# Kernel tuning notes

Hardware: AMD Instinct MI355X
Metric: run time of the kernel (lower is better)

The kernel has to match this reference:

```python
import jax, jax.numpy as jnp
import numpy as np

DIM = 64          # d_model
D_INNER = 128     # 2 * DIM (mamba expand=2)
D_STATE = 16
D_CONV = 4
DT_RANK = 4       # ceil(DIM / 16)


def setup_inputs() -> dict:
    key = jax.random.key(0)
    ks = jax.random.split(key, 8)
    s = 0.05
    f32 = jnp.float32
    return {
        "x": jax.random.normal(ks[0], (2, DIM, 96, 96), f32),
        # GroupNorm(1, dim)
        "gn_gamma": jnp.ones((DIM,), f32),
        "gn_beta": jnp.zeros((DIM,), f32),
        # Mamba params
        "W_in": (jax.random.normal(ks[1], (2 * D_INNER, DIM), f32) * s),
        "b_in": jnp.zeros((2 * D_INNER,), f32),
        "conv_w": (jax.random.normal(ks[2], (D_INNER, 1, D_CONV), f32) * s),
        "conv_b": jnp.zeros((D_INNER,), f32),
        "W_xproj": (jax.random.normal(ks[3], (DT_RANK + 2 * D_STATE, D_INNER), f32) * s),
        "W_dt": (jax.random.normal(ks[4], (D_INNER, DT_RANK), f32) * s),
        "b_dt": jnp.full((D_INNER,), -4.6, f32),  # softplus(-4.6) ~ 0.01
        "A_log": jnp.log(jnp.broadcast_to(jnp.arange(1, D_STATE + 1, dtype=f32), (D_INNER, D_STATE))),
        "Dp": jnp.ones((D_INNER,), f32),
        "W_out": (jax.random.normal(ks[5], (DIM, D_INNER), f32) * s),
        "b_out": jnp.zeros((DIM,), f32),
        # proj: Conv2d(dim, dim, 1) + BatchNorm2d(dim) eval-mode + GELU
        "proj_w": (jax.random.normal(ks[6], (DIM, DIM), f32) * s),
        "proj_b": jnp.zeros((DIM,), f32),
        "bn_gamma": jnp.ones((DIM,), f32),
        "bn_beta": jnp.zeros((DIM,), f32),
        "bn_mean": jnp.zeros((DIM,), f32),
        "bn_var": jnp.ones((DIM,), f32),
    }


def _mamba(u, W_in, b_in, conv_w, conv_b, W_xproj, W_dt, b_dt, A_log, Dp, W_out, b_out):
    # u: [B, L, DIM]
    xz = u @ W_in.T + b_in                      # [B, L, 2*D_INNER]
    x, z = jnp.split(xz, 2, axis=-1)            # each [B, L, D_INNER]
    # depthwise causal conv over L
    xc = jnp.transpose(x, (0, 2, 1))            # [B, D_INNER, L]
    xc = jax.lax.conv_general_dilated(
        xc, conv_w, (1,), [(D_CONV - 1, 0)],
        dimension_numbers=("NCH", "OIH", "NCH"), feature_group_count=D_INNER)
    x = jax.nn.silu(jnp.transpose(xc, (0, 2, 1)) + conv_b)   # [B, L, D_INNER]
    # input-dependent dt, B, C
    dbc = x @ W_xproj.T                          # [B, L, DT_RANK + 2*D_STATE]
    dt = dbc[..., :DT_RANK]
    Bm = dbc[..., DT_RANK:DT_RANK + D_STATE]     # [B, L, D_STATE]
    Cm = dbc[..., DT_RANK + D_STATE:]            # [B, L, D_STATE]
    dt = jax.nn.softplus(dt @ W_dt.T + b_dt)     # [B, L, D_INNER]
    A = -jnp.exp(A_log)                          # [D_INNER, D_STATE]
    deltaA = jnp.exp(dt[..., None] * A)                          # [B, L, D_INNER, D_STATE]
    deltaBu = dt[..., None] * Bm[:, :, None, :] * x[..., None]   # [B, L, D_INNER, D_STATE]
    # parallel linear recurrence h_t = a_t * h_{t-1} + b_t, h_0 = 0
    def comb(e1, e2):
        a1, b1 = e1
        a2, b2 = e2
        return a1 * a2, a2 * b1 + b2
    _, h = jax.lax.associative_scan(comb, (deltaA, deltaBu), axis=1)
    y = jnp.einsum("blds,bls->bld", h, Cm) + x * Dp
    y = y * jax.nn.silu(z)
    return y @ W_out.T + b_out                   # [B, L, DIM]


def reference(x, gn_gamma, gn_beta, W_in, b_in, conv_w, conv_b, W_xproj, W_dt, b_dt,
              A_log, Dp, W_out, b_out, proj_w, proj_b, bn_gamma, bn_beta, bn_mean, bn_var):
    B, C, H, W = x.shape
    # GroupNorm(1, C): normalize over (C, H, W) per sample, biased var
    mu = x.mean(axis=(1, 2, 3), keepdims=True)
    var = x.var(axis=(1, 2, 3), keepdims=True)
    xn = (x - mu) / jnp.sqrt(var + 1e-5)
    xn = xn * gn_gamma[None, :, None, None] + gn_beta[None, :, None, None]
    xn = jnp.clip(xn, -10.0, 10.0)
    res = xn
    seq = jnp.transpose(xn, (0, 2, 3, 1)).reshape(B, H * W, C)
    y = _mamba(seq, W_in, b_in, conv_w, conv_b, W_xproj, W_dt, b_dt, A_log, Dp, W_out, b_out)
    y2d = jnp.transpose(y.reshape(B, H, W, C), (0, 3, 1, 2))
    # proj: 1x1 conv + eval BatchNorm + exact GELU
    p = jnp.einsum("oc,bchw->bohw", proj_w, y2d) + proj_b[None, :, None, None]
    p = (p - bn_mean[None, :, None, None]) / jnp.sqrt(bn_var[None, :, None, None] + 1e-5)
    p = p * bn_gamma[None, :, None, None] + bn_beta[None, :, None, None]
    p = jax.nn.gelu(p, approximate=False)
    return jnp.clip(res + p, -10.0, 10.0)
```

## Files before the change

kernel.cpp:

```cpp
#include <hip/hip_runtime.h>
#include <math.h>

#define DIMC 64
#define DIN  128
#define LSEQ 9216
#define NPB  (DIMC*LSEQ)
#define NCH  192
#define CTL  48
#define NCHAIN 4096
#define PADR 132

__device__ __forceinline__ float siluf(float v)    { return v / (1.f + __expf(-v)); }
__device__ __forceinline__ float softplusf(float v){ return (v > 20.f) ? v : log1pf(__expf(v)); }
__device__ __forceinline__ float clip10(float v)   { return fminf(10.f, fmaxf(-10.f, v)); }

__global__ void k_reduce(const float* __restrict__ x, float* __restrict__ sums) {
  int b = blockIdx.y;
  const float* xb = x + (size_t)b * NPB;
  float s = 0.f, s2 = 0.f;
  for (int i = blockIdx.x * blockDim.x + threadIdx.x; i < NPB; i += gridDim.x * blockDim.x) {
    float v = xb[i]; s += v; s2 = fmaf(v, v, s2);
  }
  __shared__ float l1[256], l2[256];
  int t = threadIdx.x;
  l1[t] = s; l2[t] = s2; __syncthreads();
  for (int off = 128; off > 0; off >>= 1) {
    if (t < off) { l1[t] += l1[t + off]; l2[t] += l2[t + off]; }
    __syncthreads();
  }
  if (t == 0) { atomicAdd(&sums[2*b], l1[0]); atomicAdd(&sums[2*b+1], l2[0]); }
}

__global__ void k_norm(const float* __restrict__ x, const float* __restrict__ gam,
                       const float* __restrict__ bet, const float* __restrict__ sums,
                       float* __restrict__ seq, float* __restrict__ res) {
  int b = blockIdx.y, l0 = blockIdx.x * 64;
  float mean = sums[2*b] * (1.f / NPB);
  float var  = sums[2*b+1] * (1.f / NPB) - mean * mean;
  float inv  = rsqrtf(var + 1e-5f);
  __shared__ float tile[64][65];
  int t = threadIdx.x;
  int lr = t & 63, cg = t >> 6;
  #pragma unroll
  for (int i = 0; i < 16; i++) {
    int c = i * 4 + cg;
    size_t idx = ((size_t)(b * DIMC + c)) * LSEQ + l0 + lr;
    float v = x[idx];
    v = (v - mean) * inv * gam[c] + bet[c];
    v = clip10(v);
    res[idx] = v;
    tile[c][lr] = v;
  }
  __syncthreads();
  int cc = t & 63, lg = t >> 6;
  #pragma unroll
  for (int i = 0; i < 16; i++) {
    int l = i * 4 + lg;
    seq[((size_t)(b * LSEQ + l0 + l)) * DIMC + cc] = tile[cc][l];
  }
}

__global__ void k_prep(const float* __restrict__ W_in, const float* __restrict__ proj_w,
                       const float* __restrict__ W_out, const float* __restrict__ b_out,
                       const float* __restrict__ proj_b,
                       float* __restrict__ Wt, float* __restrict__ Mt, float* __restrict__ bp) {
  int i = blockIdx.x * 256 + threadIdx.x;
  if (i < 16384) {
    int k = i >> 8, c = i & 255;
    Wt[i] = W_in[c * 64 + k];
    return;
  }
  int j = i - 16384;
  if (j < 8192) {
    int d = j >> 6, o = j & 63;
    float a = 0.f;
    for (int c = 0; c < 64; c++) a = fmaf(proj_w[o * 64 + c], W_out[c * DIN + d], a);
    Mt[j] = a;
    return;
  }
  int k2 = i - 24576;
  if (k2 < 64) {
    float a = proj_b[k2];
    for (int c = 0; c < 64; c++) a = fmaf(proj_w[k2 * 64 + c], b_out[c], a);
    bp[k2] = a;
  }
}

__global__ void k_inproj(const float* __restrict__ seq, const float* __restrict__ Wt,
                         const float* __restrict__ b_in,
                         float* __restrict__ xo, float* __restrict__ zo) {
  int row0 = blockIdx.x * 16;
  int c = threadIdx.x;
  float acc[16];
  float bi = b_in[c];
  #pragma unroll
  for (int r = 0; r < 16; r++) acc[r] = bi;
  const float* sp = seq + (size_t)row0 * DIMC;
  #pragma unroll 4
  for (int k = 0; k < 64; k++) {
    float w = Wt[k * 256 + c];
    #pragma unroll
    for (int r = 0; r < 16; r++) acc[r] = fmaf(w, sp[r * 64 + k], acc[r]);
  }
  #pragma unroll
  for (int r = 0; r < 16; r++) {
    size_t rr = (size_t)(row0 + r);
    if (c < DIN) xo[rr * DIN + c] = acc[r];
    else         zo[rr * DIN + (c - DIN)] = acc[r];
  }
}

__global__ void k_conv_proj(const float* __restrict__ x, const float* __restrict__ conv_w,
                            const float* __restrict__ conv_b, const float* __restrict__ W_xproj,
                            const float* __restrict__ W_dt, const float* __restrict__ b_dt,
                            float* __restrict__ xs, float* __restrict__ dt,
                            float* __restrict__ Bm, float* __restrict__ Cm) {
  int b = blockIdx.y, l0 = blockIdx.x * 64;
  __shared__ float xt[67 * PADR];
  __shared__ float red[4 * 64 * 37];
  __shared__ float dt4[64 * 4];
  int t = threadIdx.x;

  for (int i = t; i < 67 * 128; i += 256) {
    int lr = i >> 7, d = i & 127;
    int l = l0 - 3 + lr;
    xt[lr * PADR + d] = (l >= 0) ? x[((size_t)b * LSEQ + l) * DIN + d] : 0.f;
  }
  __syncthreads();

  int q = t >> 6;
  int qu = __builtin_amdgcn_readfirstlane(q);
  int lr = t & 63;
  size_t row = (size_t)b * LSEQ + l0 + lr;
  const float* xtr = xt + lr * PADR + qu * 32;
  const float4* cw4 = (const float4*)conv_w;
  const float4* cb4 = (const float4*)conv_b;
  float xv[32];
  #pragma unroll
  for (int c = 0; c < 8; c++) {
    int dbase = qu * 32 + c * 4;
    float4 t0 = *(const float4*)(xtr + 0 * PADR + c * 4);
    float4 t1 = *(const float4*)(xtr + 1 * PADR + c * 4);
    float4 t2 = *(const float4*)(xtr + 2 * PADR + c * 4);
    float4 t3 = *(const float4*)(xtr + 3 * PADR + c * 4);
    float4 cb = cb4[qu * 8 + c];
    float4 w;
    float a0, a1, a2, a3;
    w = cw4[dbase + 0];
    a0 = cb.x; a0 = fmaf(t0.x, w.x, a0); a0 = fmaf(t1.x, w.y, a0);
    a0 = fmaf(t2.x, w.z, a0); a0 = fmaf(t3.x, w.w, a0); a0 = siluf(a0);
    w = cw4[dbase + 1];
    a1 = cb.y; a1 = fmaf(t0.y, w.x, a1); a1 = fmaf(t1.y, w.y, a1);
    a1 = fmaf(t2.y, w.z, a1); a1 = fmaf(t3.y, w.w, a1); a1 = siluf(a1);
    w = cw4[dbase + 2];
    a2 = cb.z; a2 = fmaf(t0.z, w.x, a2); a2 = fmaf(t1.z, w.y, a2);
    a2 = fmaf(t2.z, w.z, a2); a2 = fmaf(t3.z, w.w, a2); a2 = siluf(a2);
    w = cw4[dbase + 3];
    a3 = cb.w; a3 = fmaf(t0.w, w.x, a3); a3 = fmaf(t1.w, w.y, a3);
    a3 = fmaf(t2.w, w.z, a3); a3 = fmaf(t3.w, w.w, a3); a3 = siluf(a3);
    xv[c * 4 + 0] = a0; xv[c * 4 + 1] = a1; xv[c * 4 + 2] = a2; xv[c * 4 + 3] = a3;
    *(float4*)(xs + row * DIN + dbase) = make_float4(a0, a1, a2, a3);
  }

  const float4* W4 = (const float4*)W_xproj;
  float* myred = red + (q * 64 + lr) * 37;
  for (int j = 0; j < 36; j++) {
    const float4* wr = W4 + j * 32 + qu * 8;
    float p0 = 0.f, p1 = 0.f;
    #pragma unroll
    for (int c = 0; c < 8; c += 2) {
      float4 w0 = wr[c], w1 = wr[c + 1];
      p0 = fmaf(xv[c * 4 + 0], w0.x, p0);
      p0 = fmaf(xv[c * 4 + 1], w0.y, p0);
      p0 = fmaf(xv[c * 4 + 2], w0.z, p0);
      p0 = fmaf(xv[c * 4 + 3], w0.w, p0);
      p1 = fmaf(xv[c * 4 + 4], w1.x, p1);
      p1 = fmaf(xv[c * 4 + 5], w1.y, p1);
      p1 = fmaf(xv[c * 4 + 6], w1.z, p1);
      p1 = fmaf(xv[c * 4 + 7], w1.w, p1);
    }
    myred[j] = p0 + p1;
  }
  __syncthreads();

  for (int k = 0; k < 9; k++) {
    int task = t + k * 256;
    int lrr = task / 36, j = task - lrr * 36;
    int o = lrr * 37 + j;
    float ssum = red[o] + red[2368 + o] + red[2 * 2368 + o] + red[3 * 2368 + o];
    size_t rrow = (size_t)b * LSEQ + l0 + lrr;
    if (j < 4)       dt4[lrr * 4 + j] = ssum;
    else if (j < 20) Bm[rrow * 16 + (j - 4)]  = ssum;
    else             Cm[rrow * 16 + (j - 20)] = ssum;
  }
  __syncthreads();

  int lr2 = t >> 2, q2 = t & 3;
  float4 dv = *(const float4*)(dt4 + lr2 * 4);
  size_t rrow = (size_t)b * LSEQ + l0 + lr2;
  const float4* Wd4 = (const float4*)W_dt;
  const float4* bd4 = (const float4*)b_dt;
  #pragma unroll
  for (int c = 0; c < 8; c++) {
    int dd = q2 * 32 + c * 4;
    float4 bb = bd4[q2 * 8 + c];
    float4 w;
    float s0, s1, s2, s3;
    w = Wd4[dd + 0];
    s0 = bb.x; s0 = fmaf(dv.x, w.x, s0); s0 = fmaf(dv.y, w.y, s0);
    s0 = fmaf(dv.z, w.z, s0); s0 = fmaf(dv.w, w.w, s0);
    w = Wd4[dd + 1];
    s1 = bb.y; s1 = fmaf(dv.x, w.x, s1); s1 = fmaf(dv.y, w.y, s1);
    s1 = fmaf(dv.z, w.z, s1); s1 = fmaf(dv.w, w.w, s1);
    w = Wd4[dd + 2];
    s2 = bb.z; s2 = fmaf(dv.x, w.x, s2); s2 = fmaf(dv.y, w.y, s2);
    s2 = fmaf(dv.z, w.z, s2); s2 = fmaf(dv.w, w.w, s2);
    w = Wd4[dd + 3];
    s3 = bb.w; s3 = fmaf(dv.x, w.x, s3); s3 = fmaf(dv.y, w.y, s3);
    s3 = fmaf(dv.z, w.z, s3); s3 = fmaf(dv.w, w.w, s3);
    *(float4*)(dt + rrow * DIN + dd) =
        make_float4(softplusf(s0), softplusf(s1), softplusf(s2), softplusf(s3));
  }
}

__global__ void __launch_bounds__(512) k_scanA(
    const float* __restrict__ dt, const float* __restrict__ Bmat,
    const float* __restrict__ xs, const float* __restrict__ A_log,
    float* __restrict__ Ap, float* __restrict__ Bg) {
  int chunk = blockIdx.x, b = blockIdx.y;
  int t = threadIdx.x;
  int d = t >> 2, q = t & 3;
  const float* al = A_log + d * 16 + q * 4;
  float a0 = -__expf(al[0]), a1 = -__expf(al[1]);
  float a2 = -__expf(al[2]), a3 = -__expf(al[3]);
  size_t base = (size_t)b * LSEQ + (size_t)chunk * CTL;
  const float* dtp = dt + base * DIN + d;
  const float* xsp = xs + base * DIN + d;
  const float4* bp4 = (const float4*)(Bmat + base * 16 + q * 4);
  float h0 = 0.f, h1 = 0.f, h2 = 0.f, h3 = 0.f;
  float p0 = 1.f, p1 = 1.f, p2 = 1.f, p3 = 1.f;
  #pragma unroll 4
  for (int i = 0; i < CTL; i++) {
    float dtv = dtp[(size_t)i * DIN];
    float xv  = xsp[(size_t)i * DIN];
    float4 bA = bp4[i * 4];
    float u = dtv * xv;
    float e;
    e = __expf(dtv * a0); h0 = fmaf(e, h0, u * bA.x); p0 *= e;
    e = __expf(dtv * a1); h1 = fmaf(e, h1, u * bA.y); p1 *= e;
    e = __expf(dtv * a2); h2 = fmaf(e, h2, u * bA.z); p2 *= e;
    e = __expf(dtv * a3); h3 = fmaf(e, h3, u * bA.w); p3 *= e;
  }
  size_t idx = (size_t)chunk * NCHAIN + (size_t)(b * DIN + d) * 16 + q * 4;
  *(float4*)(Ap + idx) = make_float4(p0, p1, p2, p3);
  *(float4*)(Bg + idx) = make_float4(h0, h1, h2, h3);
}

__global__ void k_scanB(const float* __restrict__ Ap, const float* __restrict__ Bg,
                        float* __restrict__ hinit) {
  int chain = blockIdx.x * 64 + threadIdx.x;
  float h = 0.f;
  for (int c = 0; c < NCH; c++) {
    size_t idx = (size_t)c * NCHAIN + chain;
    hinit[idx] = h;
    h = fmaf(Ap[idx], h, Bg[idx]);
  }
}

__global__ void __launch_bounds__(512) k_scanC(
    const float* __restrict__ dt, const float* __restrict__ Bmat,
    const float* __restrict__ Cmat, const float* __restrict__ xs,
    const float* __restrict__ z, const float* __restrict__ A_log,
    const float* __restrict__ Dp, const float* __restrict__ hinit,
    float* __restrict__ y) {
  int chunk = blockIdx.x, b = blockIdx.y;
  int t = threadIdx.x;
  int d = t >> 2, q = t & 3;
  const float* al = A_log + d * 16 + q * 4;
  float a0 = -__expf(al[0]), a1 = -__expf(al[1]);
  float a2 = -__expf(al[2]), a3 = -__expf(al[3]);
  float dp = Dp[d];
  size_t base = (size_t)b * LSEQ + (size_t)chunk * CTL;
  const float* dtp = dt + base * DIN + d;
  const float* xsp = xs + base * DIN + d;
  const float* zp  = z  + base * DIN + d;
  float* yp        = y  + base * DIN + d;
  const float4* bp4 = (const float4*)(Bmat + base * 16 + q * 4);
  const float4* cp4 = (const float4*)(Cmat + base * 16 + q * 4);
  size_t idx = (size_t)chunk * NCHAIN + (size_t)(b * DIN + d) * 16 + q * 4;
  float4 hv = *(const float4*)(hinit + idx);
  float h0 = hv.x, h1 = hv.y, h2 = hv.z, h3 = hv.w;
  #pragma unroll 2
  for (int i = 0; i < CTL; i++) {
    float dtv = dtp[(size_t)i * DIN];
    float xv  = xsp[(size_t)i * DIN];
    float4 bA = bp4[i * 4];
    float4 cA = cp4[i * 4];
    float u = dtv * xv;
    float e, p;
    e = __expf(dtv * a0); h0 = fmaf(e, h0, u * bA.x); p  = h0 * cA.x;
    e = __expf(dtv * a1); h1 = fmaf(e, h1, u * bA.y); p  = fmaf(h1, cA.y, p);
    e = __expf(dtv * a2); h2 = fmaf(e, h2, u * bA.z); p  = fmaf(h2, cA.z, p);
    e = __expf(dtv * a3); h3 = fmaf(e, h3, u * bA.w); p  = fmaf(h3, cA.w, p);
    p += __shfl_xor(p, 1);
    p += __shfl_xor(p, 2);
    if (q == 0) {
      float zv = zp[(size_t)i * DIN];
      yp[(size_t)i * DIN] = (p + xv * dp) * siluf(zv);
    }
  }
}

__global__ void k_out(const float* __restrict__ y, const float* __restrict__ Mt,
                      const float* __restrict__ bp, const float* __restrict__ bn_g,
                      const float* __restrict__ bn_bt, const float* __restrict__ bn_m,
                      const float* __restrict__ bn_v, const float* __restrict__ res,
                      float* __restrict__ out) {
  int b = blockIdx.y, l0 = blockIdx.x * 64;
  int t = threadIdx.x;
  int c = t & 63, lg = t >> 6;
  __shared__ float tile[64][65];
  float acc[16];
  float bpc = bp[c];
  #pragma unroll
  for (int i = 0; i < 16; i++) acc[i] = bpc;
  const float* yb = y + ((size_t)b * LSEQ + l0 + lg * 16) * DIN;
  #pragma unroll 4
  for (int d = 0; d < DIN; d++) {
    float m = Mt[d * 64 + c];
    #pragma unroll
    for (int i = 0; i < 16; i++) acc[i] = fmaf(m, yb[i * DIN + d], acc[i]);
  }
  float g = bn_g[c], bt = bn_bt[c], mu = bn_m[c];
  float iv = rsqrtf(bn_v[c] + 1e-5f);
  #pragma unroll
  for (int i = 0; i < 16; i++) {
    float a = (acc[i] - mu) * iv * g + bt;
    a = 0.5f * a * (1.f + erff(a * 0.70710678118654752f));
    tile[c][lg * 16 + i] = a;
  }
  __syncthreads();
  int l = t & 63, cg = t >> 6;
  #pragma unroll
  for (int i = 0; i < 16; i++) {
    int cc = cg * 16 + i;
    size_t idx = ((size_t)(b * DIMC + cc)) * LSEQ + l0 + l;
    out[idx] = clip10(res[idx] + tile[cc][l]);
  }
}

extern "C" void kernel_launch(void* const* d_in, const int* in_sizes, int n_in,
                              void* d_out, int out_size, void* d_ws, size_t ws_size,
                              hipStream_t stream) {
  const float* x       = (const float*)d_in[0];
  const float* gn_g    = (const float*)d_in[1];
  const float* gn_b    = (const float*)d_in[2];
  const float* W_in    = (const float*)d_in[3];
  const float* b_in    = (const float*)d_in[4];
  const float* conv_w  = (const float*)d_in[5];
  const float* conv_b  = (const float*)d_in[6];
  const float* W_xproj = (const float*)d_in[7];
  const float* W_dt    = (const float*)d_in[8];
  const float* b_dt    = (const float*)d_in[9];
  const float* A_log   = (const float*)d_in[10];
  const float* Dp      = (const float*)d_in[11];
  const float* W_out   = (const float*)d_in[12];
  const float* b_out   = (const float*)d_in[13];
  const float* proj_w  = (const float*)d_in[14];
  const float* proj_b  = (const float*)d_in[15];
  const float* bn_g    = (const float*)d_in[16];
  const float* bn_bt   = (const float*)d_in[17];
  const float* bn_m    = (const float*)d_in[18];
  const float* bn_v    = (const float*)d_in[19];

  float* ws = (float*)d_ws;
  float* sums = ws;
  float* seq  = ws + 64;
  float* res  = seq + 1179648;
  float* xbuf = res + 1179648;
  float* zbuf = xbuf + 2359296;
  float* xsb  = zbuf + 2359296;
  float* dtb  = xsb + 2359296;
  float* Bmb  = dtb + 2359296;
  float* Cmb  = Bmb + 294912;
  float* Wt   = Cmb + 294912;
  float* Mt   = Wt + 16384;
  float* bp   = Mt + 8192;
  float* Bgb  = bp + 64;
  float* hib  = Bgb + 786432;
  float* Apb  = seq;
  float* ybuf = xbuf;

  hipMemsetAsync(sums, 0, 64 * sizeof(float), stream);

  k_reduce<<<dim3(256, 2), 256, 0, stream>>>(x, sums);
  k_prep<<<97, 256, 0, stream>>>(W_in, proj_w, W_out, b_out, proj_b, Wt, Mt, bp);
  k_norm<<<dim3(144, 2), 256, 0, stream>>>(x, gn_g, gn_b, sums, seq, res);
  k_inproj<<<1152, 256, 0, stream>>>(seq, Wt, b_in, xbuf, zbuf);
  k_conv_proj<<<dim3(144, 2), 256, 0, stream>>>(xbuf, conv_w, conv_b, W_xproj, W_dt, b_dt,
                                                xsb, dtb, Bmb, Cmb);
  k_scanA<<<dim3(NCH, 2), 512, 0, stream>>>(dtb, Bmb, xsb, A_log, Apb, Bgb);
  k_scanB<<<64, 64, 0, stream>>>(Apb, Bgb, hib);
  k_scanC<<<dim3(NCH, 2), 512, 0, stream>>>(dtb, Bmb, Cmb, xsb, zbuf, A_log, Dp, hib, ybuf);
  k_out<<<dim3(144, 2), 256, 0, stream>>>(ybuf, Mt, bp, bn_g, bn_bt, bn_m, bn_v, res,
                                          (float*)d_out);
}
```

Before: 289.9 us.

## Fuse causal conv into in-projection and fold dt projection into x-proj weights

The depthwise causal conv and SiLU now run inside the in-projection kernel, which recomputes three halo rows per 16-row tile so the pre-conv x buffer never goes to global memory. The low-rank dt path (W_xproj rows times W_dt) is precomputed in the prep kernel into a single 128x160 weight matrix. A new x-proj kernel then produces dt, B and C with one GEMM-style pass plus softplus, removing the shared-memory reduction and the second dt stage. The cost is about 19/16 redundant in-projection work for the halo, and a different summation order for dt. At l0==0 the halo rows are zeroed to keep the conv causal padding correct.

New measurement: 284.3 us. Within noise of the previous version (-1.9%).

```diff
diff --git a/kernel.cpp b/kernel.cpp
--- a/kernel.cpp
+++ b/kernel.cpp
@@ -8,7 +8,6 @@
 #define NCH  192
 #define CTL  48
 #define NCHAIN 4096
-#define PADR 132
 
 __device__ __forceinline__ float siluf(float v)    { return v / (1.f + __expf(-v)); }
 __device__ __forceinline__ float softplusf(float v){ return (v > 20.f) ? v : log1pf(__expf(v)); }
@@ -62,8 +61,10 @@
 
 __global__ void k_prep(const float* __restrict__ W_in, const float* __restrict__ proj_w,
                        const float* __restrict__ W_out, const float* __restrict__ b_out,
-                       const float* __restrict__ proj_b,
-                       float* __restrict__ Wt, float* __restrict__ Mt, float* __restrict__ bp) {
+                       const float* __restrict__ proj_b, const float* __restrict__ W_xproj,
+                       const float* __restrict__ W_dt, const float* __restrict__ b_dt,
+                       float* __restrict__ Wt, float* __restrict__ Mt, float* __restrict__ bp,
+                       float* __restrict__ Wbt, float* __restrict__ bbig) {
   int i = blockIdx.x * 256 + threadIdx.x;
   if (i < 16384) {
     int k = i >> 8, c = i & 255;
@@ -78,148 +79,133 @@
     Mt[j] = a;
     return;
   }
-  int k2 = i - 24576;
+  int k2 = j - 8192;
   if (k2 < 64) {
     float a = proj_b[k2];
     for (int c = 0; c < 64; c++) a = fmaf(proj_w[k2 * 64 + c], b_out[c], a);
     bp[k2] = a;
-  }
-}
-
-__global__ void k_inproj(const float* __restrict__ seq, const float* __restrict__ Wt,
-                         const float* __restrict__ b_in,
-                         float* __restrict__ xo, float* __restrict__ zo) {
+    return;
+  }
+  int m = j - 8256;
+  if (m < 20480) {
+    int k = m / 160, c = m - k * 160;
+    float v;
+    if (c < 128) {
+      v = 0.f;
+      #pragma unroll
+      for (int r = 0; r < 4; r++) v = fmaf(W_dt[c * 4 + r], W_xproj[r * DIN + k], v);
+    } else {
+      v = W_xproj[(c - 124) * DIN + k];
+    }
+    Wbt[m] = v;
+    return;
+  }
+  int c3 = m - 20480;
+  if (c3 < 160) bbig[c3] = (c3 < 128) ? b_dt[c3] : 0.f;
+}
+
+__global__ void k_inproj_conv(const float* __restrict__ seq, const float* __restrict__ Wt,
+                              const float* __restrict__ b_in, const float* __restrict__ conv_w,
+                              const float* __restrict__ conv_b,
+                              float* __restrict__ xs, float* __restrict__ zo) {
   int row0 = blockIdx.x * 16;
-  int c = threadIdx.x;
-  float acc[16];
+  int l0 = row0 % LSEQ;
+  int t = threadIdx.x;
+  __shared__ float sq[19 * 64];
+  for (int i = t; i < 19 * 16; i += 256) {
+    int r = i >> 4, k4 = i & 15;
+    int rr = row0 - 3 + r; if (rr < 0) rr = 0;
+    *(float4*)(sq + r * 64 + k4 * 4) = *(const float4*)(seq + (size_t)rr * DIMC + k4 * 4);
+  }
+  __syncthreads();
+
+  int c = t;
   float bi = b_in[c];
-  #pragma unroll
-  for (int r = 0; r < 16; r++) acc[r] = bi;
-  const float* sp = seq + (size_t)row0 * DIMC;
+  float a[19];
+  #pragma unroll
+  for (int r = 0; r < 19; r++) a[r] = bi;
+  const float4* sq4 = (const float4*)sq;
   #pragma unroll 4
-  for (int k = 0; k < 64; k++) {
-    float w = Wt[k * 256 + c];
-    #pragma unroll
-    for (int r = 0; r < 16; r++) acc[r] = fmaf(w, sp[r * 64 + k], acc[r]);
-  }
-  #pragma unroll
-  for (int r = 0; r < 16; r++) {
-    size_t rr = (size_t)(row0 + r);
-    if (c < DIN) xo[rr * DIN + c] = acc[r];
-    else         zo[rr * DIN + (c - DIN)] = acc[r];
-  }
-}
-
-__global__ void k_conv_proj(const float* __restrict__ x, const float* __restrict__ conv_w,
-                            const float* __restrict__ conv_b, const float* __restrict__ W_xproj,
-                            const float* __restrict__ W_dt, const float* __restrict__ b_dt,
-                            float* __restrict__ xs, float* __restrict__ dt,
-                            float* __restrict__ Bm, float* __restrict__ Cm) {
-  int b = blockIdx.y, l0 = blockIdx.x * 64;
-  __shared__ float xt[67 * PADR];
-  __shared__ float red[4 * 64 * 37];
-  __shared__ float dt4[64 * 4];
-  int t = threadIdx.x;
-
-  for (int i = t; i < 67 * 128; i += 256) {
-    int lr = i >> 7, d = i & 127;
-    int l = l0 - 3 + lr;
-    xt[lr * PADR + d] = (l >= 0) ? x[((size_t)b * LSEQ + l) * DIN + d] : 0.f;
+  for (int k4 = 0; k4 < 16; k4++) {
+    float w0 = Wt[(k4 * 4 + 0) * 256 + c];
+    float w1 = Wt[(k4 * 4 + 1) * 256 + c];
+    float w2 = Wt[(k4 * 4 + 2) * 256 + c];
+    float w3 = Wt[(k4 * 4 + 3) * 256 + c];
+    #pragma unroll
+    for (int r = 0; r < 19; r++) {
+      float4 v = sq4[r * 16 + k4];
+      a[r] = fmaf(w0, v.x, a[r]);
+      a[r] = fmaf(w1, v.y, a[r]);
+      a[r] = fmaf(w2, v.z, a[r]);
+      a[r] = fmaf(w3, v.w, a[r]);
+    }
+  }
+  if (c < DIN) {
+    if (l0 == 0) { a[0] = 0.f; a[1] = 0.f; a[2] = 0.f; }
+    float4 cw = *(const float4*)(conv_w + c * 4);
+    float cb = conv_b[c];
+    #pragma unroll
+    for (int i = 0; i < 16; i++) {
+      float v = cb;
+      v = fmaf(a[i + 0], cw.x, v);
+      v = fmaf(a[i + 1], cw.y, v);
+      v = fmaf(a[i + 2], cw.z, v);
+      v = fmaf(a[i + 3], cw.w, v);
+      xs[(size_t)(row0 + i) * DIN + c] = siluf(v);
+    }
+  } else {
+    int cz = c - DIN;
+    #pragma unroll
+    for (int i = 0; i < 16; i++) zo[(size_t)(row0 + i) * DIN + cz] = a[i + 3];
+  }
+}
+
+__global__ void k_xproj(const float* __restrict__ xs, const float* __restrict__ Wbt,
+                        const float* __restrict__ bbig,
+                        float* __restrict__ dt, float* __restrict__ Bm, float* __restrict__ Cm) {
+  int row0 = blockIdx.x * 16;
+  int t = threadIdx.x;
+  __shared__ float xt[16 * DIN];
+  for (int i = t; i < 16 * 32; i += 320) {
+    int r = i >> 5, k4 = i & 31;
+    *(float4*)(xt + r * DIN + k4 * 4) = *(const float4*)(xs + (size_t)(row0 + r) * DIN + k4 * 4);
   }
   __syncthreads();
 
-  int q = t >> 6;
-  int qu = __builtin_amdgcn_readfirstlane(q);
-  int lr = t & 63;
-  size_t row = (size_t)b * LSEQ + l0 + lr;
-  const float* xtr = xt + lr * PADR + qu * 32;
-  const float4* cw4 = (const float4*)conv_w;
-  const float4* cb4 = (const float4*)conv_b;
-  float xv[32];
-  #pragma unroll
-  for (int c = 0; c < 8; c++) {
-    int dbase = qu * 32 + c * 4;
-    float4 t0 = *(const float4*)(xtr + 0 * PADR + c * 4);
-    float4 t1 = *(const float4*)(xtr + 1 * PADR + c * 4);
-    float4 t2 = *(const float4*)(xtr + 2 * PADR + c * 4);
-    float4 t3 = *(const float4*)(xtr + 3 * PADR + c * 4);
-    float4 cb = cb4[qu * 8 + c];
-    float4 w;
-    float a0, a1, a2, a3;
-    w = cw4[dbase + 0];
-    a0 = cb.x; a0 = fmaf(t0.x, w.x, a0); a0 = fmaf(t1.x, w.y, a0);
-    a0 = fmaf(t2.x, w.z, a0); a0 = fmaf(t3.x, w.w, a0); a0 = siluf(a0);
-    w = cw4[dbase + 1];
-    a1 = cb.y; a1 = fmaf(t0.y, w.x, a1); a1 = fmaf(t1.y, w.y, a1);
-    a1 = fmaf(t2.y, w.z, a1); a1 = fmaf(t3.y, w.w, a1); a1 = siluf(a1);
-    w = cw4[dbase + 2];
-    a2 = cb.z; a2 = fmaf(t0.z, w.x, a2); a2 = fmaf(t1.z, w.y, a2);
-    a2 = fmaf(t2.z, w.z, a2); a2 = fmaf(t3.z, w.w, a2); a2 = siluf(a2);
-    w = cw4[dbase + 3];
-    a3 = cb.w; a3 = fmaf(t0.w, w.x, a3); a3 = fmaf(t1.w, w.y, a3);
-    a3 = fmaf(t2.w, w.z, a3); a3 = fmaf(t3.w, w.w, a3); a3 = siluf(a3);
-    xv[c * 4 + 0] = a0; xv[c * 4 + 1] = a1; xv[c * 4 + 2] = a2; xv[c * 4 + 3] = a3;
-    *(float4*)(xs + row * DIN + dbase) = make_float4(a0, a1, a2, a3);
-  }
-
-  const float4* W4 = (const float4*)W_xproj;
-  float* myred = red + (q * 64 + lr) * 37;
-  for (int j = 0; j < 36; j++) {
-    const float4* wr = W4 + j * 32 + qu * 8;
-    float p0 = 0.f, p1 = 0.f;
-    #pragma unroll
-    for (int c = 0; c < 8; c += 2) {
-      float4 w0 = wr[c], w1 = wr[c + 1];
-      p0 = fmaf(xv[c * 4 + 0], w0.x, p0);
-      p0 = fmaf(xv[c * 4 + 1], w0.y, p0);
-      p0 = fmaf(xv[c * 4 + 2], w0.z, p0);
-      p0 = fmaf(xv[c * 4 + 3], w0.w, p0);
-      p1 = fmaf(xv[c * 4 + 4], w1.x, p1);
-      p1 = fmaf(xv[c * 4 + 5], w1.y, p1);
-      p1 = fmaf(xv[c * 4 + 6], w1.z, p1);
-      p1 = fmaf(xv[c * 4 + 7], w1.w, p1);
-    }
-    myred[j] = p0 + p1;
-  }
-  __syncthreads();
-
-  for (int k = 0; k < 9; k++) {
-    int task = t + k * 256;
-    int lrr = task / 36, j = task - lrr * 36;
-    int o = lrr * 37 + j;
-    float ssum = red[o] + red[2368 + o] + red[2 * 2368 + o] + red[3 * 2368 + o];
-    size_t rrow = (size_t)b * LSEQ + l0 + lrr;
-    if (j < 4)       dt4[lrr * 4 + j] = ssum;
-    else if (j < 20) Bm[rrow * 16 + (j - 4)]  = ssum;
-    else             Cm[rrow * 16 + (j - 20)] = ssum;
-  }
-  __syncthreads();
-
-  int lr2 = t >> 2, q2 = t & 3;
-  float4 dv = *(const float4*)(dt4 + lr2 * 4);
-  size_t rrow = (size_t)b * LSEQ + l0 + lr2;
-  const float4* Wd4 = (const float4*)W_dt;
-  const float4* bd4 = (const float4*)b_dt;
-  #pragma unroll
-  for (int c = 0; c < 8; c++) {
-    int dd = q2 * 32 + c * 4;
-    float4 bb = bd4[q2 * 8 + c];
-    float4 w;
-    float s0, s1, s2, s3;
-    w = Wd4[dd + 0];
-    s0 = bb.x; s0 = fmaf(dv.x, w.x, s0); s0 = fmaf(dv.y, w.y, s0);
-    s0 = fmaf(dv.z, w.z, s0); s0 = fmaf(dv.w, w.w, s0);
-    w = Wd4[dd + 1];
-    s1 = bb.y; s1 = fmaf(dv.x, w.x, s1); s1 = fmaf(dv.y, w.y, s1);
-    s1 = fmaf(dv.z, w.z, s1); s1 = fmaf(dv.w, w.w, s1);
-    w = Wd4[dd + 2];
-    s2 = bb.z; s2 = fmaf(dv.x, w.x, s2); s2 = fmaf(dv.y, w.y, s2);
-    s2 = fmaf(dv.z, w.z, s2); s2 = fmaf(dv.w, w.w, s2);
-    w = Wd4[dd + 3];
-    s3 = bb.w; s3 = fmaf(dv.x, w.x, s3); s3 = fmaf(dv.y, w.y, s3);
-    s3 = fmaf(dv.z, w.z, s3); s3 = fmaf(dv.w, w.w, s3);
-    *(float4*)(dt + rrow * DIN + dd) =
-        make_float4(softplusf(s0), softplusf(s1), softplusf(s2), softplusf(s3));
+  int c = (t < 160) ? t : t - 160;
+  int rbase = (t < 160) ? 0 : 8;
+  float acc[8];
+  float bb = bbig[c];
+  #pragma unroll
+  for (int r = 0; r < 8; r++) acc[r] = bb;
+  const float4* xt4 = (const float4*)(xt + rbase * DIN);
+  #pragma unroll 2
+  for (int k4 = 0; k4 < 32; k4++) {
+    float w0 = Wbt[(k4 * 4 + 0) * 160 + c];
+    float w1 = Wbt[(k4 * 4 + 1) * 160 + c];
+    float w2 = Wbt[(k4 * 4 + 2) * 160 + c];
+    float w3 = Wbt[(k4 * 4 + 3) * 160 + c];
+    #pragma unroll
+    for (int r = 0; r < 8; r++) {
+      float4 v = xt4[r * 32 + k4];
+      acc[r] = fmaf(w0, v.x, acc[r]);
+      acc[r] = fmaf(w1, v.y, acc[r]);
+      acc[r] = fmaf(w2, v.z, acc[r]);
+      acc[r] = fmaf(w3, v.w, acc[r]);
+    }
+  }
+  if (c < 128) {
+    #pragma unroll
+    for (int r = 0; r < 8; r++)
+      dt[(size_t)(row0 + rbase + r) * DIN + c] = softplusf(acc[r]);
+  } else if (c < 144) {
+    #pragma unroll
+    for (int r = 0; r < 8; r++)
+      Bm[(size_t)(row0 + rbase + r) * 16 + (c - 128)] = acc[r];
+  } else {
+    #pragma unroll
+    for (int r = 0; r < 8; r++)
+      Cm[(size_t)(row0 + rbase + r) * 16 + (c - 144)] = acc[r];
   }
 }
 
@@ -377,8 +363,8 @@
   float* sums = ws;
   float* seq  = ws + 64;
   float* res  = seq + 1179648;
-  float* xbuf = res + 1179648;
-  float* zbuf = xbuf + 2359296;
+  float* ybuf = res + 1179648;
+  float* zbuf = ybuf + 2359296;
   float* xsb  = zbuf + 2359296;
   float* dtb  = xsb + 2359296;
   float* Bmb  = dtb + 2359296;
@@ -386,19 +372,20 @@
   float* Wt   = Cmb + 294912;
   float* Mt   = Wt + 16384;
   float* bp   = Mt + 8192;
-  float* Bgb  = bp + 64;
+  float* Wbt  = bp + 64;
+  float* bbig = Wbt + 20480;
+  float* Bgb  = bbig + 160;
   float* hib  = Bgb + 786432;
   float* Apb  = seq;
-  float* ybuf = xbuf;
 
   hipMemsetAsync(sums, 0, 64 * sizeof(float), stream);
 
   k_reduce<<<dim3(256, 2), 256, 0, stream>>>(x, sums);
-  k_prep<<<97, 256, 0, stream>>>(W_in, proj_w, W_out, b_out, proj_b, Wt, Mt, bp);
+  k_prep<<<177, 256, 0, stream>>>(W_in, proj_w, W_out, b_out, proj_b, W_xproj, W_dt, b_dt,
+                                  Wt, Mt, bp, Wbt, bbig);
   k_norm<<<dim3(144, 2), 256, 0, stream>>>(x, gn_g, gn_b, sums, seq, res);
-  k_inproj<<<1152, 256, 0, stream>>>(seq, Wt, b_in, xbuf, zbuf);
-  k_conv_proj<<<dim3(144, 2), 256, 0, stream>>>(xbuf, conv_w, conv_b, W_xproj, W_dt, b_dt,
-                                                xsb, dtb, Bmb, Cmb);
+  k_inproj_conv<<<1152, 256, 0, stream>>>(seq, Wt, b_in, conv_w, conv_b, xsb, zbuf);
+  k_xproj<<<1152, 320, 0, stream>>>(xsb, Wbt, bbig, dtb, Bmb, Cmb);
   k_scanA<<<dim3(NCH, 2), 512, 0, stream>>>(dtb, Bmb, xsb, A_log, Apb, Bgb);
   k_scanB<<<64, 64, 0, stream>>>(Apb, Bgb, hib);
   k_scanC<<<dim3(NCH, 2), 512, 0, stream>>>(dtb, Bmb, Cmb, xsb, zbuf, A_log, Dp, hib, ybuf);
```
